# Kernel optimization log

Measured on AMD Instinct MI355X. Metric: run time of the kernel, lower is better.

The kernel has to match this reference:

```python
import jax, jax.numpy as jnp
import numpy as np

N = 50000
E = 800000
IN_CH = 128
HID = 64
HEADS = 4
EPS = 1e-5
NEG_SLOPE = 0.2


def _gat_conv(x, src, dst, W, a_src, a_dst, b, heads, out_ch, concat):
    n = x.shape[0]
    h = (x @ W).reshape(n, heads, out_ch)                      # [N,H,C]
    alpha_src = jnp.sum(h * a_src, axis=-1)                    # [N,H]
    alpha_dst = jnp.sum(h * a_dst, axis=-1)                    # [N,H]
    e = jax.nn.leaky_relu(alpha_src[src] + alpha_dst[dst], NEG_SLOPE)  # [E',H]
    # segment softmax over incoming edges of each destination node
    m = jax.ops.segment_max(e, dst, num_segments=n)            # [N,H]
    e = jnp.exp(e - m[dst])
    denom = jax.ops.segment_sum(e, dst, num_segments=n)        # [N,H]
    alpha = e / denom[dst]                                     # [E',H]
    msg = h[src] * alpha[:, :, None]                           # [E',H,C]
    out = jax.ops.segment_sum(msg, dst, num_segments=n)        # [N,H,C]
    if concat:
        out = out.reshape(n, heads * out_ch)
    else:
        out = out.mean(axis=1)
    return out + b


def _bn_eval(x, gamma, beta, mean, var):
    return (x - mean) * (gamma / jnp.sqrt(var + EPS)) + beta


def setup_inputs() -> dict:
    key = jax.random.key(0)
    ks = jax.random.split(key, 24)
    s = 0.1
    x = jax.random.normal(ks[0], (N, IN_CH), dtype=jnp.float32)
    edge_index = jax.random.randint(ks[1], (2, E), 0, N, dtype=jnp.int32)
    d0, d1 = IN_CH, HID * HEADS
    inp = {
        'x': x, 'edge_index': edge_index,
        # layer 0: in_ch -> hidden, heads=4, concat
        'W0': jax.random.normal(ks[2], (d0, HEADS * HID), jnp.float32) * s,
        'as0': jax.random.normal(ks[3], (HEADS, HID), jnp.float32) * s,
        'ad0': jax.random.normal(ks[4], (HEADS, HID), jnp.float32) * s,
        'b0': jax.random.normal(ks[5], (HEADS * HID,), jnp.float32) * s,
        # layer 1: hidden*heads -> hidden, heads=4, concat
        'W1': jax.random.normal(ks[6], (d1, HEADS * HID), jnp.float32) * s,
        'as1': jax.random.normal(ks[7], (HEADS, HID), jnp.float32) * s,
        'ad1': jax.random.normal(ks[8], (HEADS, HID), jnp.float32) * s,
        'b1': jax.random.normal(ks[9], (HEADS * HID,), jnp.float32) * s,
        # layer 2: hidden*heads -> 1, heads=1, no concat
        'W2': jax.random.normal(ks[10], (d1, 1), jnp.float32) * s,
        'as2': jax.random.normal(ks[11], (1, 1), jnp.float32) * s,
        'ad2': jax.random.normal(ks[12], (1, 1), jnp.float32) * s,
        'b2': jax.random.normal(ks[13], (1,), jnp.float32) * s,
        # batchnorm (eval) params for the two hidden layers
        'g0': jnp.ones((d1,), jnp.float32),
        'be0': jnp.zeros((d1,), jnp.float32),
        'm0': jax.random.normal(ks[14], (d1,), jnp.float32) * s,
        'v0': jnp.ones((d1,), jnp.float32),
        'g1': jnp.ones((d1,), jnp.float32),
        'be1': jnp.zeros((d1,), jnp.float32),
        'm1': jax.random.normal(ks[15], (d1,), jnp.float32) * s,
        'v1': jnp.ones((d1,), jnp.float32),
    }
    return inp


def reference(x, edge_index, W0, as0, ad0, b0, W1, as1, ad1, b1,
              W2, as2, ad2, b2, g0, be0, m0, v0, g1, be1, m1, v1):
    n = x.shape[0]
    loops = jnp.arange(n, dtype=edge_index.dtype)
    src = jnp.concatenate([edge_index[0], loops])  # add self-loops (PyG default)
    dst = jnp.concatenate([edge_index[1], loops])

    # layer 0 (no residual: shapes differ)
    h = _gat_conv(x, src, dst, W0, as0, ad0, b0, HEADS, HID, True)
    h = jax.nn.elu(_bn_eval(h, g0, be0, m0, v0))

    # layer 1 (residual: shapes match)
    res = h
    h = _gat_conv(h, src, dst, W1, as1, ad1, b1, HEADS, HID, True)
    h = jax.nn.elu(_bn_eval(h, g1, be1, m1, v1)) + res

    # output layer: heads=1, concat=False -> [N,1]
    out = _gat_conv(h, src, dst, W2, as2, ad2, b2, 1, 1, False)
    return out.squeeze(-1)
```

## Files before the change

kernel.cpp:

```cpp
#include <hip/hip_runtime.h>
#include <math.h>

#define NEG_SLOPE 0.2f
#define BN_EPS 1e-5f

typedef __attribute__((ext_vector_type(8))) short bf16x8;
typedef __attribute__((ext_vector_type(4))) float f32x4;

static __device__ __forceinline__ unsigned short f2bf(float f){
    unsigned u = __float_as_uint(f);
    u += 0x7FFFu + ((u >> 16) & 1u);
    return (unsigned short)(u >> 16);
}
static __device__ __forceinline__ float bf2f(unsigned short v){
    return __uint_as_float((unsigned)v << 16);
}

static __device__ __forceinline__ void repack_one(const float* __restrict__ W,
    unsigned short* __restrict__ whi, unsigned short* __restrict__ wlo, int o)
{
    const int j = o & 7, ln = (o >> 3) & 63, ct = (o >> 9) & 15, kt = o >> 13;
    const int k = kt * 32 + 8 * (ln >> 4) + j;
    const int col = ct * 16 + (ln & 15);
    const float v = W[k * 256 + col];
    const unsigned short hb = f2bf(v);
    whi[o] = hb; wlo[o] = f2bf(v - bf2f(hb));
}

__global__ void prep_kernel(const float* __restrict__ W0,
    unsigned short* __restrict__ w0hi, unsigned short* __restrict__ w0lo,
    const float* __restrict__ W1,
    unsigned short* __restrict__ w1hi, unsigned short* __restrict__ w1lo,
    int* __restrict__ deg, int N)
{
    const int bid = blockIdx.x, t = threadIdx.x;
    if (bid < 128){
        repack_one(W0, w0hi, w0lo, bid * 256 + t);
    } else if (bid < 384){
        repack_one(W1, w1hi, w1lo, (bid - 128) * 256 + t);
    } else {
        const int i = (bid - 384) * 256 + t;
        if (i < N) deg[i] = 1;
    }
}

__global__ __launch_bounds__(256) void mfma_gemm0(
    const float* __restrict__ x,
    const unsigned short* __restrict__ wbhi, const unsigned short* __restrict__ wblo,
    const float* __restrict__ a_s, const float* __restrict__ a_d,
    unsigned short* __restrict__ hout,
    float* __restrict__ asrc, float* __restrict__ adst, int N)
{
    constexpr int K = 128;
    const int t = threadIdx.x, lane = t & 63, wid = t >> 6;
    const int n0 = blockIdx.x * 64;
    const int l15 = lane & 15, lg = lane >> 4;

    const float* ap[4];
#pragma unroll
    for (int rt = 0; rt < 4; ++rt){
        int node = n0 + rt * 16 + l15;
        if (node > N - 1) node = N - 1;
        ap[rt] = &x[(size_t)node * K + 8 * lg];
    }
    const unsigned short* bph = &wbhi[((size_t)(wid * 4) * 64 + lane) * 8];
    const unsigned short* bpl = &wblo[((size_t)(wid * 4) * 64 + lane) * 8];

    f32x4 acc[4][4];
#pragma unroll
    for (int rt = 0; rt < 4; ++rt)
#pragma unroll
        for (int q = 0; q < 4; ++q) acc[rt][q] = (f32x4){0.f, 0.f, 0.f, 0.f};

#pragma unroll 2
    for (int kt = 0; kt < K / 32; ++kt){
        bf16x8 bhi[4], blo[4];
#pragma unroll
        for (int q = 0; q < 4; ++q){
            bhi[q] = *(const bf16x8*)(bph + ((size_t)kt * 16 + q) * 512);
            blo[q] = *(const bf16x8*)(bpl + ((size_t)kt * 16 + q) * 512);
        }
        float4 f0[4], f1[4];
#pragma unroll
        for (int rt = 0; rt < 4; ++rt){
            f0[rt] = *(const float4*)(ap[rt] + kt * 32);
            f1[rt] = *(const float4*)(ap[rt] + kt * 32 + 4);
        }
        bf16x8 ahi[4], alo[4];
#pragma unroll
        for (int rt = 0; rt < 4; ++rt){
            const float fv[8] = {f0[rt].x, f0[rt].y, f0[rt].z, f0[rt].w,
                                 f1[rt].x, f1[rt].y, f1[rt].z, f1[rt].w};
#pragma unroll
            for (int j = 0; j < 8; ++j){
                const unsigned short hb = f2bf(fv[j]);
                ahi[rt][j] = (short)hb;
                alo[rt][j] = (short)f2bf(fv[j] - bf2f(hb));
            }
        }
#pragma unroll
        for (int q = 0; q < 4; ++q)
#pragma unroll
            for (int rt = 0; rt < 4; ++rt){
                acc[rt][q] = __builtin_amdgcn_mfma_f32_16x16x32_bf16(ahi[rt], bhi[q], acc[rt][q], 0, 0, 0);
                acc[rt][q] = __builtin_amdgcn_mfma_f32_16x16x32_bf16(alo[rt], bhi[q], acc[rt][q], 0, 0, 0);
                acc[rt][q] = __builtin_amdgcn_mfma_f32_16x16x32_bf16(ahi[rt], blo[q], acc[rt][q], 0, 0, 0);
            }
    }

    float avs[4], avd[4];
#pragma unroll
    for (int q = 0; q < 4; ++q){
        avs[q] = a_s[wid * 64 + q * 16 + l15];
        avd[q] = a_d[wid * 64 + q * 16 + l15];
    }
    float sp[4][4], dp[4][4];
#pragma unroll
    for (int rt = 0; rt < 4; ++rt){
#pragma unroll
        for (int reg = 0; reg < 4; ++reg){
            const int node = n0 + rt * 16 + lg * 4 + reg;
            float s = 0.f, d = 0.f;
            unsigned short hv[4];
#pragma unroll
            for (int q = 0; q < 4; ++q){
                const float v = acc[rt][q][reg];
                s = fmaf(v, avs[q], s); d = fmaf(v, avd[q], d);
                hv[q] = f2bf(v);
            }
            if (node < N){
#pragma unroll
                for (int q = 0; q < 4; ++q)
                    hout[(size_t)node * 256 + (wid * 4 + q) * 16 + l15] = hv[q];
            }
            sp[rt][reg] = s; dp[rt][reg] = d;
        }
    }
#pragma unroll
    for (int off = 1; off <= 8; off <<= 1){
#pragma unroll
        for (int rt = 0; rt < 4; ++rt)
#pragma unroll
            for (int reg = 0; reg < 4; ++reg){
                sp[rt][reg] += __shfl_xor(sp[rt][reg], off, 64);
                dp[rt][reg] += __shfl_xor(dp[rt][reg], off, 64);
            }
    }
    if (l15 == 0){
#pragma unroll
        for (int rt = 0; rt < 4; ++rt)
#pragma unroll
            for (int reg = 0; reg < 4; ++reg){
                const int node = n0 + rt * 16 + lg * 4 + reg;
                if (node < N){
                    asrc[(size_t)node * 4 + wid] = sp[rt][reg];
                    adst[(size_t)node * 4 + wid] = dp[rt][reg];
                }
            }
    }
}

__global__ __launch_bounds__(256) void mfma_gemm1(
    const unsigned short* __restrict__ xb,
    const unsigned short* __restrict__ wbhi, const unsigned short* __restrict__ wblo,
    const float* __restrict__ a_s, const float* __restrict__ a_d,
    unsigned short* __restrict__ hout,
    float* __restrict__ asrc, float* __restrict__ adst, int N)
{
    constexpr int K = 256;
    const int t = threadIdx.x, lane = t & 63, wid = t >> 6;
    const int n0 = blockIdx.x * 64;
    const int l15 = lane & 15, lg = lane >> 4;

    const unsigned short* ap[4];
#pragma unroll
    for (int rt = 0; rt < 4; ++rt){
        int node = n0 + rt * 16 + l15;
        if (node > N - 1) node = N - 1;
        ap[rt] = &xb[(size_t)node * K + 8 * lg];
    }
    const unsigned short* bph = &wbhi[((size_t)(wid * 4) * 64 + lane) * 8];
    const unsigned short* bpl = &wblo[((size_t)(wid * 4) * 64 + lane) * 8];

    f32x4 acc[4][4];
#pragma unroll
    for (int rt = 0; rt < 4; ++rt)
#pragma unroll
        for (int q = 0; q < 4; ++q) acc[rt][q] = (f32x4){0.f, 0.f, 0.f, 0.f};

#pragma unroll 2
    for (int kt = 0; kt < K / 32; ++kt){
        bf16x8 bhi[4], blo[4];
#pragma unroll
        for (int q = 0; q < 4; ++q){
            bhi[q] = *(const bf16x8*)(bph + ((size_t)kt * 16 + q) * 512);
            blo[q] = *(const bf16x8*)(bpl + ((size_t)kt * 16 + q) * 512);
        }
        bf16x8 a[4];
#pragma unroll
        for (int rt = 0; rt < 4; ++rt)
            a[rt] = *(const bf16x8*)(ap[rt] + kt * 32);

#pragma unroll
        for (int q = 0; q < 4; ++q)
#pragma unroll
            for (int rt = 0; rt < 4; ++rt){
                acc[rt][q] = __builtin_amdgcn_mfma_f32_16x16x32_bf16(a[rt], bhi[q], acc[rt][q], 0, 0, 0);
                acc[rt][q] = __builtin_amdgcn_mfma_f32_16x16x32_bf16(a[rt], blo[q], acc[rt][q], 0, 0, 0);
            }
    }

    float avs[4], avd[4];
#pragma unroll
    for (int q = 0; q < 4; ++q){
        avs[q] = a_s[wid * 64 + q * 16 + l15];
        avd[q] = a_d[wid * 64 + q * 16 + l15];
    }
    float sp[4][4], dp[4][4];
#pragma unroll
    for (int rt = 0; rt < 4; ++rt){
#pragma unroll
        for (int reg = 0; reg < 4; ++reg){
            const int node = n0 + rt * 16 + lg * 4 + reg;
            float s = 0.f, d = 0.f;
            unsigned short hv[4];
#pragma unroll
            for (int q = 0; q < 4; ++q){
                const float v = acc[rt][q][reg];
                s = fmaf(v, avs[q], s); d = fmaf(v, avd[q], d);
                hv[q] = f2bf(v);
            }
            if (node < N){
#pragma unroll
                for (int q = 0; q < 4; ++q)
                    hout[(size_t)node * 256 + (wid * 4 + q) * 16 + l15] = hv[q];
            }
            sp[rt][reg] = s; dp[rt][reg] = d;
        }
    }
#pragma unroll
    for (int off = 1; off <= 8; off <<= 1){
#pragma unroll
        for (int rt = 0; rt < 4; ++rt)
#pragma unroll
            for (int reg = 0; reg < 4; ++reg){
                sp[rt][reg] += __shfl_xor(sp[rt][reg], off, 64);
                dp[rt][reg] += __shfl_xor(dp[rt][reg], off, 64);
            }
    }
    if (l15 == 0){
#pragma unroll
        for (int rt = 0; rt < 4; ++rt)
#pragma unroll
            for (int reg = 0; reg < 4; ++reg){
                const int node = n0 + rt * 16 + lg * 4 + reg;
                if (node < N){
                    asrc[(size_t)node * 4 + wid] = sp[rt][reg];
                    adst[(size_t)node * 4 + wid] = dp[rt][reg];
                }
            }
    }
}

__global__ void deg_hist_kernel(const int* __restrict__ ei, int E, int* __restrict__ deg){
    int e = blockIdx.x * blockDim.x + threadIdx.x;
    if (e < E) atomicAdd(&deg[ei[E + e]], 1);
}

__global__ __launch_bounds__(256) void part_sum_kernel(const int* __restrict__ deg,
                                                       int* __restrict__ bsum, int N)
{
    __shared__ int red[256];
    const int t = threadIdx.x;
    const int i0 = blockIdx.x * 1024 + t * 4;
    int s = 0;
    if (i0 + 3 < N){
        const int4 v = *(const int4*)&deg[i0];
        s = v.x + v.y + v.z + v.w;
    } else {
#pragma unroll
        for (int j = 0; j < 4; ++j) if (i0 + j < N) s += deg[i0 + j];
    }
    red[t] = s; __syncthreads();
    for (int off = 128; off >= 1; off >>= 1){
        if (t < off) red[t] += red[t + off];
        __syncthreads();
    }
    if (t == 0) bsum[blockIdx.x] = red[0];
}

__global__ __launch_bounds__(256) void scan_part_kernel(int* __restrict__ bsum, int nb,
                                                        int* __restrict__ row, int N)
{
    __shared__ int sh[256];
    const int t = threadIdx.x;
    const int v = (t < nb) ? bsum[t] : 0;
    sh[t] = v; __syncthreads();
    for (int off = 1; off < 256; off <<= 1){
        int u = (t >= off) ? sh[t - off] : 0;
        __syncthreads();
        sh[t] += u;
        __syncthreads();
    }
    if (t < nb) bsum[t] = sh[t] - v;
    if (t == nb - 1) row[N] = sh[t];
}

__global__ __launch_bounds__(256) void distribute_kernel(const int* __restrict__ deg,
    const int* __restrict__ bsum, int* __restrict__ row, int* __restrict__ cursor, int N)
{
    __shared__ int ts[256];
    const int t = threadIdx.x;
    const int i0 = blockIdx.x * 1024 + t * 4;
    int d[4]; int s = 0;
#pragma unroll
    for (int j = 0; j < 4; ++j){ d[j] = (i0 + j < N) ? deg[i0 + j] : 0; s += d[j]; }
    ts[t] = s; __syncthreads();
    for (int off = 1; off < 256; off <<= 1){
        int u = (t >= off) ? ts[t - off] : 0;
        __syncthreads();
        ts[t] += u;
        __syncthreads();
    }
    int base = bsum[blockIdx.x] + ts[t] - s;
#pragma unroll
    for (int j = 0; j < 4; ++j){
        if (i0 + j < N){ row[i0 + j] = base; cursor[i0 + j] = base; base += d[j]; }
    }
}

__global__ void scatter_kernel(const int* __restrict__ ei, int E, int N,
                               int* __restrict__ cursor, int* __restrict__ csr)
{
    int e = blockIdx.x * blockDim.x + threadIdx.x;
    if (e >= E + N) return;
    int s, d;
    if (e < E){ s = ei[e]; d = ei[E + e]; } else { s = d = e - E; }
    int pos = atomicAdd(&cursor[d], 1);
    csr[pos] = s;
}

#define DEG_CAP 128
template<bool LAST>
__global__ __launch_bounds__(256) void agg4_kernel(
    const int* __restrict__ row, const int* __restrict__ csr,
    const float* __restrict__ asrc, const float* __restrict__ adst,
    const unsigned short* __restrict__ h,
    const float* __restrict__ b, const float* __restrict__ g,
    const float* __restrict__ be, const float* __restrict__ mean,
    const float* __restrict__ var,
    const unsigned short* __restrict__ res,
    unsigned short* __restrict__ outbf,
    float* __restrict__ outh2,
    const float* __restrict__ W2,
    int N)
{
    __shared__ float plds[4][DEG_CAP * 4];
    __shared__ int   slds[4][DEG_CAP];
    const int wid = threadIdx.x >> 6, lane = threadIdx.x & 63;
    const int node = blockIdx.x * 4 + wid;
    if (node >= N) return;
    const int beg = row[node], end = row[node + 1], deg = end - beg;
    const int degc = deg < DEG_CAP ? deg : DEG_CAP;
    const int head = lane >> 4;

    const float4 ad = *(const float4*)&adst[(size_t)node * 4];

    float d0 = 0.f, d1 = 0.f, d2 = 0.f, d3 = 0.f;
    for (int i = lane; i < deg; i += 64){
        const int s = csr[beg + i];
        const float4 as = *(const float4*)&asrc[(size_t)s * 4];
        float v0 = as.x + ad.x, v1 = as.y + ad.y, v2 = as.z + ad.z, v3 = as.w + ad.w;
        v0 = v0 > 0.f ? v0 : NEG_SLOPE * v0;
        v1 = v1 > 0.f ? v1 : NEG_SLOPE * v1;
        v2 = v2 > 0.f ? v2 : NEG_SLOPE * v2;
        v3 = v3 > 0.f ? v3 : NEG_SLOPE * v3;
        const float p0 = __expf(v0), p1 = __expf(v1);
        const float p2 = __expf(v2), p3 = __expf(v3);
        d0 += p0; d1 += p1; d2 += p2; d3 += p3;
        if (i < DEG_CAP){
            *(float4*)&plds[wid][i * 4] = make_float4(p0, p1, p2, p3);
            slds[wid][i] = s << 9;
        }
    }
    for (int off = 32; off >= 1; off >>= 1){
        d0 += __shfl_xor(d0, off, 64); d1 += __shfl_xor(d1, off, 64);
        d2 += __shfl_xor(d2, off, 64); d3 += __shfl_xor(d3, off, 64);
    }

    float a0 = 0.f, a1 = 0.f, a2 = 0.f, a3 = 0.f;
    {
        const char* hb = (const char*)h + lane * 8;
        const float* pb = &plds[wid][0];
        const int* sb = &slds[wid][0];
#define EDGE_BODY(slot)                                                        \
        {                                                                      \
            const float p_ = pb[(slot) * 4 + head];                            \
            const ushort4 hv_ = *(const ushort4*)(hb + sb[slot]);              \
            a0 = fmaf(p_, bf2f(hv_.x), a0); a1 = fmaf(p_, bf2f(hv_.y), a1);    \
            a2 = fmaf(p_, bf2f(hv_.z), a2); a3 = fmaf(p_, bf2f(hv_.w), a3);    \
        }
        int i = 0;
        for (; i + 2 <= degc; i += 2){
            EDGE_BODY(i);
            EDGE_BODY(i + 1);
        }
        for (; i < degc; ++i) EDGE_BODY(i);
#undef EDGE_BODY
    }

    for (int jj = beg + DEG_CAP; jj < end; ++jj){
        const int s = csr[jj];
        const float4 as = *(const float4*)&asrc[(size_t)s * 4];
        float e0 = as.x + ad.x, e1 = as.y + ad.y, e2 = as.z + ad.z, e3 = as.w + ad.w;
        float eh = (head == 0) ? e0 : (head == 1) ? e1 : (head == 2) ? e2 : e3;
        eh = eh > 0.f ? eh : NEG_SLOPE * eh;
        const float p = __expf(eh);
        const ushort4 hv = *(const ushort4*)&h[(size_t)s * 256 + lane * 4];
        a0 = fmaf(p, bf2f(hv.x), a0); a1 = fmaf(p, bf2f(hv.y), a1);
        a2 = fmaf(p, bf2f(hv.z), a2); a3 = fmaf(p, bf2f(hv.w), a3);
    }

    const int l15 = lane & 15;
    const float dsel = (head == 0) ? d0 : (head == 1) ? d1 : (head == 2) ? d2 : d3;
    const float rdi = 1.f / dsel;
    const int c0 = head * 64 + 4 * l15;
    const float4 bv  = *(const float4*)&b[c0];
    const float4 gv  = *(const float4*)&g[c0];
    const float4 bev = *(const float4*)&be[c0];
    const float4 mv  = *(const float4*)&mean[c0];
    const float4 vv4 = *(const float4*)&var[c0];
    const float ava[4]  = {a0, a1, a2, a3};
    const float bva[4]  = {bv.x, bv.y, bv.z, bv.w};
    const float gva[4]  = {gv.x, gv.y, gv.z, gv.w};
    const float beva[4] = {bev.x, bev.y, bev.z, bev.w};
    const float mva[4]  = {mv.x, mv.y, mv.z, mv.w};
    const float vva[4]  = {vv4.x, vv4.y, vv4.z, vv4.w};
    float rh[4] = {0.f, 0.f, 0.f, 0.f};
    if (LAST){
        const ushort4 rv = *(const ushort4*)&res[(size_t)node * 256 + c0];
        rh[0] = bf2f(rv.x); rh[1] = bf2f(rv.y); rh[2] = bf2f(rv.z); rh[3] = bf2f(rv.w);
    }
    float vvv[4];
#pragma unroll
    for (int j = 0; j < 4; ++j){
        float v = ava[j] * rdi + bva[j];
        v = (v - mva[j]) * (gva[j] * rsqrtf(vva[j] + BN_EPS)) + beva[j];
        v = v > 0.f ? v : (__expf(v) - 1.f);
        vvv[j] = v + rh[j];
    }
    if (!LAST){
        ushort4 o4;
        o4.x = f2bf(vvv[0]); o4.y = f2bf(vvv[1]);
        o4.z = f2bf(vvv[2]); o4.w = f2bf(vvv[3]);
        *(ushort4*)&outbf[(size_t)node * 256 + c0] = o4;
    } else {
        const float4 w2v = *(const float4*)&W2[c0];
        float part = vvv[0] * w2v.x + vvv[1] * w2v.y + vvv[2] * w2v.z + vvv[3] * w2v.w;
        for (int off = 32; off >= 1; off >>= 1) part += __shfl_xor(part, off, 64);
        if (lane == 0) outh2[node] = part;
    }
}

__global__ void agg2_kernel(const int* __restrict__ row, const int* __restrict__ csr,
                            const float* __restrict__ h2,
                            const float* __restrict__ as2, const float* __restrict__ ad2,
                            const float* __restrict__ b2, float* __restrict__ out, int N)
{
    const int n = blockIdx.x * blockDim.x + threadIdx.x;
    if (n >= N) return;
    const float A_s = as2[0];
    const float hd  = h2[n] * ad2[0];
    const int beg = row[n], end = row[n + 1];
    float den = 0.f, acc = 0.f;
    for (int i = beg; i < end; ++i){
        const float hv = h2[csr[i]];
        float a = fmaf(A_s, hv, hd);
        a = a > 0.f ? a : NEG_SLOPE * a;
        const float p = __expf(a);
        den += p; acc = fmaf(p, hv, acc);
    }
    out[n] = acc / den + b2[0];
}

extern "C" void kernel_launch(void* const* d_in, const int* in_sizes, int n_in,
                              void* d_out, int out_size, void* d_ws, size_t ws_size,
                              hipStream_t stream)
{
    const float* x   = (const float*)d_in[0];
    const int*   ei  = (const int*)  d_in[1];
    const float* W0  = (const float*)d_in[2];
    const float* as0 = (const float*)d_in[3];
    const float* ad0 = (const float*)d_in[4];
    const float* b0  = (const float*)d_in[5];
    const float* W1  = (const float*)d_in[6];
    const float* as1 = (const float*)d_in[7];
    const float* ad1 = (const float*)d_in[8];
    const float* b1  = (const float*)d_in[9];
    const float* W2  = (const float*)d_in[10];
    const float* as2 = (const float*)d_in[11];
    const float* ad2 = (const float*)d_in[12];
    const float* b2  = (const float*)d_in[13];
    const float* g0  = (const float*)d_in[14];
    const float* be0 = (const float*)d_in[15];
    const float* m0  = (const float*)d_in[16];
    const float* v0  = (const float*)d_in[17];
    const float* g1  = (const float*)d_in[18];
    const float* be1 = (const float*)d_in[19];
    const float* m1  = (const float*)d_in[20];
    const float* v1  = (const float*)d_in[21];

    const int N = in_sizes[0] / 128;
    const int E = in_sizes[1] / 2;
    const int EN = E + N;

    char* w = (char*)d_ws;
    unsigned short* H    = (unsigned short*)w;  w += (size_t)N * 256 * 2;
    unsigned short* P0   = (unsigned short*)w;  w += (size_t)N * 256 * 2;
    float*    asrc   = (float*)w;   w += (size_t)N * 4 * 4;
    float*    adst   = (float*)w;   w += (size_t)N * 4 * 4;
    int*      deg    = (int*)w;     w += (size_t)N * 4;
    int*      cursor = (int*)w;     w += (size_t)N * 4;
    int*      csr    = (int*)w;     w += (size_t)EN * 4;
    float*    h2     = (float*)w;   w += (size_t)N * 4;
    int*      bsum   = (int*)w;     w += 1024;
    unsigned short* Wb0hi = (unsigned short*)w; w += (size_t)128 * 256 * 2;
    unsigned short* Wb0lo = (unsigned short*)w; w += (size_t)128 * 256 * 2;
    unsigned short* Wb1hi = (unsigned short*)w; w += (size_t)256 * 256 * 2;
    unsigned short* Wb1lo = (unsigned short*)w; w += (size_t)256 * 256 * 2;
    int*      rowp   = (int*)w;     w += (size_t)(N + 1) * 4;

    const int gN64  = (N + 63) / 64;
    const int gN4   = (N + 3) / 4;
    const int gNt   = (N + 255) / 256;
    const int gE    = (E + 255) / 256;
    const int gEN   = (EN + 255) / 256;
    const int nb    = (N + 1023) / 1024;

    prep_kernel<<<384 + gNt, 256, 0, stream>>>(W0, Wb0hi, Wb0lo, W1, Wb1hi, Wb1lo, deg, N);
    deg_hist_kernel<<<gE, 256, 0, stream>>>(ei, E, deg);
    part_sum_kernel<<<nb, 256, 0, stream>>>(deg, bsum, N);
    scan_part_kernel<<<1, 256, 0, stream>>>(bsum, nb, rowp, N);
    distribute_kernel<<<nb, 256, 0, stream>>>(deg, bsum, rowp, cursor, N);
    scatter_kernel<<<gEN, 256, 0, stream>>>(ei, E, N, cursor, csr);

    mfma_gemm0<<<gN64, 256, 0, stream>>>(x, Wb0hi, Wb0lo,
                                         as0, ad0, H, asrc, adst, N);
    agg4_kernel<false><<<gN4, 256, 0, stream>>>(rowp, csr, asrc, adst, H,
                                                b0, g0, be0, m0, v0,
                                                nullptr, P0, nullptr, nullptr, N);

    mfma_gemm1<<<gN64, 256, 0, stream>>>(P0, Wb1hi, Wb1lo,
                                         as1, ad1, H, asrc, adst, N);
    agg4_kernel<true><<<gN4, 256, 0, stream>>>(rowp, csr, asrc, adst, H,
                                               b1, g1, be1, m1, v1,
                                               P0, nullptr, h2, W2, N);

    agg2_kernel<<<gNt, 256, 0, stream>>>(rowp, csr, h2, as2, ad2, b2, (float*)d_out, N);
}
```

Baseline: 324.7 us.

## Stage GEMM A tiles via global_load_lds and drop the low-part A MFMA

New measurement: 306.0 us. 5.8% less time.

```diff
diff --git a/kernel.cpp b/kernel.cpp
--- a/kernel.cpp
+++ b/kernel.cpp
@@ -14,6 +14,12 @@
 }
 static __device__ __forceinline__ float bf2f(unsigned short v){
     return __uint_as_float((unsigned)v << 16);
+}
+
+static __device__ __forceinline__ void gload_lds16(const void* g, void* l){
+    __builtin_amdgcn_global_load_lds(
+        (const __attribute__((address_space(1))) void*)g,
+        (__attribute__((address_space(3))) void*)l, 16, 0, 0);
 }
 
 static __device__ __forceinline__ void repack_one(const float* __restrict__ W,
@@ -52,17 +58,11 @@
     float* __restrict__ asrc, float* __restrict__ adst, int N)
 {
     constexpr int K = 128;
+    __shared__ float xaf[4][2][64][4];
     const int t = threadIdx.x, lane = t & 63, wid = t >> 6;
     const int n0 = blockIdx.x * 64;
     const int l15 = lane & 15, lg = lane >> 4;
 
-    const float* ap[4];
-#pragma unroll
-    for (int rt = 0; rt < 4; ++rt){
-        int node = n0 + rt * 16 + l15;
-        if (node > N - 1) node = N - 1;
-        ap[rt] = &x[(size_t)node * K + 8 * lg];
-    }
     const unsigned short* bph = &wbhi[((size_t)(wid * 4) * 64 + lane) * 8];
     const unsigned short* bpl = &wblo[((size_t)(wid * 4) * 64 + lane) * 8];
 
@@ -72,38 +72,39 @@
 #pragma unroll
         for (int q = 0; q < 4; ++q) acc[rt][q] = (f32x4){0.f, 0.f, 0.f, 0.f};
 
-#pragma unroll 2
     for (int kt = 0; kt < K / 32; ++kt){
+        __syncthreads();
+#pragma unroll
+        for (int ii = 0; ii < 2; ++ii){
+            const int i = wid * 2 + ii;
+            const int rt = i >> 1, half = i & 1;
+            int node = n0 + rt * 16 + l15;
+            if (node > N - 1) node = N - 1;
+            const float* src = &x[(size_t)node * K + kt * 32 + 8 * lg + half * 4];
+            gload_lds16(src, &xaf[rt][half][0][0]);
+        }
         bf16x8 bhi[4], blo[4];
 #pragma unroll
         for (int q = 0; q < 4; ++q){
             bhi[q] = *(const bf16x8*)(bph + ((size_t)kt * 16 + q) * 512);
             blo[q] = *(const bf16x8*)(bpl + ((size_t)kt * 16 + q) * 512);
         }
-        float4 f0[4], f1[4];
+        __syncthreads();
+
+        bf16x8 ahi[4];
 #pragma unroll
         for (int rt = 0; rt < 4; ++rt){
-            f0[rt] = *(const float4*)(ap[rt] + kt * 32);
-            f1[rt] = *(const float4*)(ap[rt] + kt * 32 + 4);
-        }
-        bf16x8 ahi[4], alo[4];
-#pragma unroll
-        for (int rt = 0; rt < 4; ++rt){
-            const float fv[8] = {f0[rt].x, f0[rt].y, f0[rt].z, f0[rt].w,
-                                 f1[rt].x, f1[rt].y, f1[rt].z, f1[rt].w};
-#pragma unroll
-            for (int j = 0; j < 8; ++j){
-                const unsigned short hb = f2bf(fv[j]);
-                ahi[rt][j] = (short)hb;
-                alo[rt][j] = (short)f2bf(fv[j] - bf2f(hb));
-            }
+            const float4 f0 = *(const float4*)&xaf[rt][0][lane][0];
+            const float4 f1 = *(const float4*)&xaf[rt][1][lane][0];
+            const float fv[8] = {f0.x, f0.y, f0.z, f0.w, f1.x, f1.y, f1.z, f1.w};
+#pragma unroll
+            for (int j = 0; j < 8; ++j) ahi[rt][j] = (short)f2bf(fv[j]);
         }
 #pragma unroll
         for (int q = 0; q < 4; ++q)
 #pragma unroll
             for (int rt = 0; rt < 4; ++rt){
                 acc[rt][q] = __builtin_amdgcn_mfma_f32_16x16x32_bf16(ahi[rt], bhi[q], acc[rt][q], 0, 0, 0);
-                acc[rt][q] = __builtin_amdgcn_mfma_f32_16x16x32_bf16(alo[rt], bhi[q], acc[rt][q], 0, 0, 0);
                 acc[rt][q] = __builtin_amdgcn_mfma_f32_16x16x32_bf16(ahi[rt], blo[q], acc[rt][q], 0, 0, 0);
             }
     }
@@ -168,17 +169,11 @@
     float* __restrict__ asrc, float* __restrict__ adst, int N)
 {
     constexpr int K = 256;
+    __shared__ unsigned short xab[4][512];
     const int t = threadIdx.x, lane = t & 63, wid = t >> 6;
     const int n0 = blockIdx.x * 64;
     const int l15 = lane & 15, lg = lane >> 4;
 
-    const unsigned short* ap[4];
-#pragma unroll
-    for (int rt = 0; rt < 4; ++rt){
-        int node = n0 + rt * 16 + l15;
-        if (node > N - 1) node = N - 1;
-        ap[rt] = &xb[(size_t)node * K + 8 * lg];
-    }
     const unsigned short* bph = &wbhi[((size_t)(wid * 4) * 64 + lane) * 8];
     const unsigned short* bpl = &wblo[((size_t)(wid * 4) * 64 + lane) * 8];
 
@@ -188,18 +183,27 @@
 #pragma unroll
         for (int q = 0; q < 4; ++q) acc[rt][q] = (f32x4){0.f, 0.f, 0.f, 0.f};
 
-#pragma unroll 2
     for (int kt = 0; kt < K / 32; ++kt){
+        __syncthreads();
+        {
+            const int rt = wid;
+            int node = n0 + rt * 16 + l15;
+            if (node > N - 1) node = N - 1;
+            const unsigned short* src = &xb[(size_t)node * K + kt * 32 + 8 * lg];
+            gload_lds16(src, &xab[rt][0]);
+        }
         bf16x8 bhi[4], blo[4];
 #pragma unroll
         for (int q = 0; q < 4; ++q){
             bhi[q] = *(const bf16x8*)(bph + ((size_t)kt * 16 + q) * 512);
             blo[q] = *(const bf16x8*)(bpl + ((size_t)kt * 16 + q) * 512);
         }
+        __syncthreads();
+
         bf16x8 a[4];
 #pragma unroll
         for (int rt = 0; rt < 4; ++rt)
-            a[rt] = *(const bf16x8*)(ap[rt] + kt * 32);
+            a[rt] = *(const bf16x8*)&xab[rt][lane * 8];
 
 #pragma unroll
         for (int q = 0; q < 4; ++q)
```
